# Optimization experiments

Measured on AMD Instinct MI355X. Metric: run time of the kernel, lower is better.

## Reference

```python
import jax, jax.numpy as jnp
import numpy as np

SIG = 0.5
EPSILON = 10.0
E = float(np.e)


def setup_inputs() -> dict:
    key = jax.random.key(0)
    k1, k2, k3, k4 = jax.random.split(key, 4)
    B, S, D, K = 8, 2048, 128, 64
    features = jax.random.normal(k1, (B, S, D), dtype=jnp.float32)
    centroids = jax.random.normal(k2, (K, D), dtype=jnp.float32)
    # phi are per-class scale stats; keep strictly positive
    phi = jax.random.uniform(k3, (K,), dtype=jnp.float32, minval=0.5, maxval=1.5)
    labels = jax.random.randint(k4, (B, S), 0, K, dtype=jnp.int32)
    return {"features": features, "centroids": centroids, "phi": phi, "labels": labels}


def _proto_supcon_loss(features, centroids, phi, labels):
    B, S, D = features.shape
    K = centroids.shape[0]
    # pairwise mean-squared-error (MSELoss reduction='mean' over D):
    # d2[b,i,j] = mean_d (f[b,i,d]-f[b,j,d])^2
    sq = jnp.sum(features * features, axis=-1)  # [B,S]
    gram = jnp.einsum('bid,bjd->bij', features, features)  # [B,S,S]
    d2 = (sq[:, :, None] + sq[:, None, :] - 2.0 * gram) / D
    d2 = jnp.maximum(d2, 0.0)

    same = labels[:, :, None] == labels[:, None, :]  # [B,S,S]
    neg_mask = ~same
    neg_cnt = jnp.sum(neg_mask, axis=-1)  # [B,S]
    # negative sample term: neg_x = mean over negatives of MSE; neg_sup = x*log(x+e)
    neg_x = jnp.sum(jnp.where(neg_mask, d2, 0.0), axis=-1) / jnp.maximum(neg_cnt, 1)
    neg_sup = neg_x * jnp.log(neg_x + E)

    # positive sample term: mean over same-label j != i (0 if no other positive,
    # matching pos_dis = [0] in the original)
    eye = jnp.eye(S, dtype=bool)
    pos_mask = same & ~eye
    pos_cnt = jnp.sum(pos_mask, axis=-1)
    pos_x = jnp.sum(jnp.where(pos_mask, d2, 0.0), axis=-1) / jnp.maximum(pos_cnt, 1)

    # centroid terms: MSE(feature, centroid_k)/phi_k, [B,S,K]
    csq = jnp.sum(centroids * centroids, axis=-1)  # [K]
    cgram = jnp.einsum('bsd,kd->bsk', features, centroids)
    cd2 = (sq[:, :, None] + csq[None, None, :] - 2.0 * cgram) / D
    cd2 = jnp.maximum(cd2, 0.0) / phi[None, None, :]

    pos_cent = jnp.take_along_axis(cd2, labels[:, :, None].astype(jnp.int32), axis=2)[..., 0]  # [B,S]
    neg_cent_x = (jnp.sum(cd2, axis=-1) - pos_cent) / (K - 1)
    neg_cent_log = neg_cent_x * jnp.log(neg_cent_x + E)

    pos_spcl = SIG * pos_x + (1.0 - SIG) * pos_cent
    neg_spcl = SIG * neg_sup + (1.0 - SIG) * neg_cent_log
    per_anchor = pos_spcl - neg_spcl + EPSILON

    # anchors contribute only if they have at least one negative sample
    contrib = neg_cnt > 0
    loss = jnp.sum(jnp.where(contrib, per_anchor, 0.0)) / S
    return loss.reshape(1, 1)


def reference(features, centroids, phi, labels):
    return _proto_supcon_loss(features, centroids, phi, labels)
```

## Files before the change

### kernel.cpp

```cpp
#include <hip/hip_runtime.h>
#include <math.h>

#define B_ 8
#define S_ 2048
#define D_ 128
#define K_ 64
#define SIG_ 0.5f
#define EPS_ 10.0f
#define E_ 2.718281828459045f

__device__ __forceinline__ int remap512(int bx) {
    return ((bx & 7) << 6) | (bx >> 3);
}

__global__ void __launch_bounds__(256) k1_stats(
    const float* __restrict__ F, const int* __restrict__ L,
    float* __restrict__ fsumK, float* __restrict__ ssumK, float* __restrict__ cntK) {
    int bx = remap512(blockIdx.x);
    int k = bx & (K_ - 1);
    int b = bx >> 6;
    int tid = threadIdx.x;
    int lane = tid & 63;
    int wv = tid >> 6;

    __shared__ float redF[4][128];
    __shared__ float redS[4];
    __shared__ int   redC[4];

    const int* Lb = L + b * S_;
    const float* Fb = F + (size_t)b * S_ * D_;

    float a0 = 0.f, a1 = 0.f, q0 = 0.f, q1 = 0.f;
    int cnt = 0;
    #pragma unroll
    for (int rr = 0; rr < 8; ++rr) {
        int r = (wv << 3) + rr;
        int lbl = Lb[(r << 6) + lane];
        unsigned long long m = __ballot(lbl == k);
        cnt += (int)__popcll(m);
        while (m) {
            int i = __ffsll((long long)m) - 1;
            m &= m - 1;
            const float* row = Fb + (size_t)((r << 6) + i) * D_;
            float v0 = row[lane];
            float v1 = row[64 + lane];
            a0 += v0; q0 = fmaf(v0, v0, q0);
            a1 += v1; q1 = fmaf(v1, v1, q1);
        }
    }
    float qq = q0 + q1;
    #pragma unroll
    for (int m = 1; m < 64; m <<= 1) qq += __shfl_xor(qq, m);
    redF[wv][lane] = a0;
    redF[wv][64 + lane] = a1;
    if (lane == 0) { redS[wv] = qq; redC[wv] = cnt; }
    __syncthreads();

    if (tid < 128) {
        float s = (redF[0][tid] + redF[1][tid]) + (redF[2][tid] + redF[3][tid]);
        fsumK[(size_t)bx * D_ + tid] = s;
    }
    if (tid == 0) {
        ssumK[bx] = (redS[0] + redS[1]) + (redS[2] + redS[3]);
        cntK[bx] = (float)(redC[0] + redC[1] + redC[2] + redC[3]);
    }
}

__global__ void __launch_bounds__(256) k3_main(
    const float* __restrict__ F, const float* __restrict__ C,
    const float* __restrict__ phi, const int* __restrict__ L,
    const float* __restrict__ fsumK, const float* __restrict__ ssumK,
    const float* __restrict__ cntK, float* __restrict__ partial) {

    __shared__ float Cs[K_ * 129];
    __shared__ float4 redA[256];
    __shared__ float Fa[D_];
    __shared__ float wacc[4];
    int tid = threadIdx.x;
    int bxw = remap512(blockIdx.x);
    int b = bxw >> 6;

    {
        const float4* C4 = (const float4*)C;
        #pragma unroll
        for (int it = 0; it < 8; ++it) {
            int i = it * 256 + tid;
            float4 v = C4[i];
            float* p = &Cs[(i >> 5) * 129 + ((i & 31) << 2)];
            p[0] = v.x; p[1] = v.y; p[2] = v.z; p[3] = v.w;
        }
    }
    {
        int d4 = tid & 31, kg = tid >> 5;
        const float4* g4 = (const float4*)(fsumK + (size_t)b * K_ * D_) + (size_t)kg * 8 * 32 + d4;
        float4 s; s.x = s.y = s.z = s.w = 0.f;
        #pragma unroll
        for (int kk = 0; kk < 8; ++kk) {
            float4 v = g4[(size_t)kk * 32];
            s.x += v.x; s.y += v.y; s.z += v.z; s.w += v.w;
        }
        redA[tid] = s;
    }
    __syncthreads();
    if (tid < 32) {
        float4 a; a.x = a.y = a.z = a.w = 0.f;
        #pragma unroll
        for (int g = 0; g < 8; ++g) {
            float4 v = redA[g * 32 + tid];
            a.x += v.x; a.y += v.y; a.z += v.z; a.w += v.w;
        }
        ((float4*)Fa)[tid] = a;
    }
    __syncthreads();

    int lane = tid & 63;

    float c0 = 0.f, c1 = 0.f, c2 = 0.f, c3 = 0.f;
    #pragma unroll
    for (int dd = 0; dd < D_; dd += 4) {
        c0 = fmaf(Cs[lane * 129 + dd + 0], Cs[lane * 129 + dd + 0], c0);
        c1 = fmaf(Cs[lane * 129 + dd + 1], Cs[lane * 129 + dd + 1], c1);
        c2 = fmaf(Cs[lane * 129 + dd + 2], Cs[lane * 129 + dd + 2], c2);
        c3 = fmaf(Cs[lane * 129 + dd + 3], Cs[lane * 129 + dd + 3], c3);
    }
    float csq = (c0 + c1) + (c2 + c3);
    float phv = phi[lane];
    float ssl = ssumK[b * K_ + lane];
    float cnl = cntK[b * K_ + lane];
    float ssA = ssl;
    #pragma unroll
    for (int m = 1; m < 64; m <<= 1) ssA += __shfl_xor(ssA, m);

    int wid = __builtin_amdgcn_readfirstlane(tid) >> 6;
    int o = bxw * 4 + wid;
    int a0g = o * 8;
    const float4* F4 = (const float4*)F;

    int j_of = lane >> 3, q = lane & 7;
    int a_mine = a0g + j_of;
    int lbl_p = L[a_mine];
    const float4* fr = F4 + (size_t)a_mine * 32;
    const float4* fk = (const float4*)(fsumK + (size_t)(b * K_ + lbl_p) * D_);
    const float4* fa4 = (const float4*)Fa;

    float sq_p = 0.f, dk_p = 0.f, da_p = 0.f;
    #pragma unroll
    for (int i = 0; i < 4; ++i) {
        int dq = i * 8 + q;
        float4 fv = fr[dq];
        float4 kv = fk[dq];
        float4 av = fa4[dq];
        sq_p = fmaf(fv.x, fv.x, fmaf(fv.y, fv.y, fmaf(fv.z, fv.z, fmaf(fv.w, fv.w, sq_p))));
        dk_p = fmaf(fv.x, kv.x, fmaf(fv.y, kv.y, fmaf(fv.z, kv.z, fmaf(fv.w, kv.w, dk_p))));
        da_p = fmaf(fv.x, av.x, fmaf(fv.y, av.y, fmaf(fv.z, av.z, fmaf(fv.w, av.w, da_p))));
    }
    #pragma unroll
    for (int m = 1; m < 8; m <<= 1) {
        sq_p += __shfl_xor(sq_p, m);
        dk_p += __shfl_xor(dk_p, m);
        da_p += __shfl_xor(da_p, m);
    }

    float facc[8];
    #pragma unroll
    for (int j = 0; j < 8; ++j) facc[j] = 0.f;

    float4 fw[8], fwn[8];
    #pragma unroll
    for (int j = 0; j < 8; ++j) fw[j] = F4[(size_t)(a0g + j) * 32 + 0];

    for (int dq = 0; dq < 32; ++dq) {
        if (dq < 31) {
            #pragma unroll
            for (int j = 0; j < 8; ++j) fwn[j] = F4[(size_t)(a0g + j) * 32 + dq + 1];
        }
        int cbase = lane * 129 + (dq << 2);
        #pragma unroll
        for (int l = 0; l < 4; ++l) {
            float cs = Cs[cbase + l];
            #pragma unroll
            for (int j = 0; j < 8; ++j) {
                float fe = (l == 0) ? fw[j].x : (l == 1) ? fw[j].y : (l == 2) ? fw[j].z : fw[j].w;
                facc[j] = fmaf(fe, cs, facc[j]);
            }
        }
        #pragma unroll
        for (int j = 0; j < 8; ++j) fw[j] = fwn[j];
    }

    float acc = 0.f;
    #pragma unroll
    for (int j = 0; j < 8; ++j) {
        float sq_j = __shfl(sq_p, j * 8);
        float dk_j = __shfl(dk_p, j * 8);
        float da_j = __shfl(da_p, j * 8);
        int lbl_j = __shfl(lbl_p, j * 8);
        float cnt_j = __shfl(cnl, lbl_j);
        float ssm_j = __shfl(ssl, lbl_j);

        float cd2 = (sq_j + csq - 2.f * facc[j]) * (1.f / D_);
        cd2 = fmaxf(cd2, 0.f) / phv;

        float s_cd = cd2;
        #pragma unroll
        for (int m = 1; m < 64; m <<= 1) s_cd += __shfl_xor(s_cd, m);
        float pos_cent = __shfl(cd2, lbl_j);

        float ncx = (s_cd - pos_cent) * (1.f / (K_ - 1));
        float S_same = (cnt_j * sq_j + ssm_j - 2.f * dk_j) * (1.f / D_);
        float S_all = ((float)S_ * sq_j + ssA - 2.f * da_j) * (1.f / D_);
        float pos_x = fmaxf(S_same, 0.f) / fmaxf(cnt_j - 1.f, 1.f);
        float neg_cnt = (float)S_ - cnt_j;
        float neg_x = fmaxf(S_all - S_same, 0.f) / fmaxf(neg_cnt, 1.f);

        float neg_sup = neg_x * __logf(neg_x + E_);
        float ncl = ncx * __logf(ncx + E_);

        float pa = SIG_ * pos_x + (1.f - SIG_) * pos_cent
                 - (SIG_ * neg_sup + (1.f - SIG_) * ncl) + EPS_;
        if (neg_cnt > 0.5f) acc += pa;
    }

    if (lane == 0) wacc[wid] = acc;
    __syncthreads();

    if (tid == 0) partial[bxw] = wacc[0] + wacc[1] + wacc[2] + wacc[3];
}

__global__ void __launch_bounds__(256) k4_reduce(
    const float* __restrict__ partial, float* __restrict__ out) {
    int tid = threadIdx.x;
    int lane = tid & 63;
    int wv = tid >> 6;
    __shared__ float w[4];
    float v = partial[tid] + partial[tid + 256];
    #pragma unroll
    for (int m = 1; m < 64; m <<= 1) v += __shfl_xor(v, m);
    if (lane == 0) w[wv] = v;
    __syncthreads();
    if (tid == 0) out[0] = (w[0] + w[1] + w[2] + w[3]) * (1.0f / (float)S_);
}

extern "C" void kernel_launch(void* const* d_in, const int* in_sizes, int n_in,
                              void* d_out, int out_size, void* d_ws, size_t ws_size,
                              hipStream_t stream) {
    const float* F = (const float*)d_in[0];
    const float* C = (const float*)d_in[1];
    const float* phi = (const float*)d_in[2];
    const int* L = (const int*)d_in[3];
    float* out = (float*)d_out;

    float* ws = (float*)d_ws;
    float* fsumK = ws;
    float* ssumK = fsumK + (size_t)B_ * K_ * D_;
    float* cntK  = ssumK + B_ * K_;
    float* partial = cntK + B_ * K_;

    k1_stats<<<B_ * K_, 256, 0, stream>>>(F, L, fsumK, ssumK, cntK);
    k3_main<<<512, 256, 0, stream>>>(F, C, phi, L, fsumK, ssumK, cntK, partial);
    k4_reduce<<<1, 256, 0, stream>>>(partial, out);
}
```

Measured before the change: 28.05 us.

## Use 512-thread main blocks and precompute centroid norms in stats kernel

The main kernel now runs 256 blocks of 512 threads instead of 512 blocks of 256, so each block's centroid staging into shared memory and its fsumK prefix reduction serve twice as many anchor waves. The squared centroid norms are computed once in the stats kernel and stored in workspace, rather than being recomputed from shared memory in every block. The final reduction reads 256 partials. Fewer, larger blocks may lower occupancy or leave some of the MI355X's CUs idle.

```diff
diff --git a/kernel.cpp b/kernel.cpp
--- a/kernel.cpp
+++ b/kernel.cpp
@@ -9,13 +9,14 @@
 #define EPS_ 10.0f
 #define E_ 2.718281828459045f
 
-__device__ __forceinline__ int remap512(int bx) {
-    return ((bx & 7) << 6) | (bx >> 3);
-}
+__device__ __forceinline__ int remap512(int bx) { return ((bx & 7) << 6) | (bx >> 3); }
+__device__ __forceinline__ int remap256(int bx) { return ((bx & 7) << 5) | (bx >> 3); }
 
 __global__ void __launch_bounds__(256) k1_stats(
-    const float* __restrict__ F, const int* __restrict__ L,
-    float* __restrict__ fsumK, float* __restrict__ ssumK, float* __restrict__ cntK) {
+    const float* __restrict__ F, const float* __restrict__ C,
+    const int* __restrict__ L,
+    float* __restrict__ fsumK, float* __restrict__ ssumK, float* __restrict__ cntK,
+    float* __restrict__ csqK) {
     int bx = remap512(blockIdx.x);
     int k = bx & (K_ - 1);
     int b = bx >> 6;
@@ -64,33 +65,42 @@
         ssumK[bx] = (redS[0] + redS[1]) + (redS[2] + redS[3]);
         cntK[bx] = (float)(redC[0] + redC[1] + redC[2] + redC[3]);
     }
-}
-
-__global__ void __launch_bounds__(256) k3_main(
+    if (b == 0 && wv == 0) {
+        float x0 = C[(k << 7) + lane];
+        float x1 = C[(k << 7) + 64 + lane];
+        float cs = fmaf(x0, x0, x1 * x1);
+        #pragma unroll
+        for (int m = 1; m < 64; m <<= 1) cs += __shfl_xor(cs, m);
+        if (lane == 0) csqK[k] = cs;
+    }
+}
+
+__global__ void __launch_bounds__(512) k3_main(
     const float* __restrict__ F, const float* __restrict__ C,
     const float* __restrict__ phi, const int* __restrict__ L,
     const float* __restrict__ fsumK, const float* __restrict__ ssumK,
-    const float* __restrict__ cntK, float* __restrict__ partial) {
+    const float* __restrict__ cntK, const float* __restrict__ csqK,
+    float* __restrict__ partial) {
 
     __shared__ float Cs[K_ * 129];
     __shared__ float4 redA[256];
     __shared__ float Fa[D_];
-    __shared__ float wacc[4];
+    __shared__ float wacc[8];
     int tid = threadIdx.x;
-    int bxw = remap512(blockIdx.x);
-    int b = bxw >> 6;
+    int bxw = remap256(blockIdx.x);
+    int b = bxw >> 5;
 
     {
         const float4* C4 = (const float4*)C;
         #pragma unroll
-        for (int it = 0; it < 8; ++it) {
-            int i = it * 256 + tid;
+        for (int it = 0; it < 4; ++it) {
+            int i = it * 512 + tid;
             float4 v = C4[i];
             float* p = &Cs[(i >> 5) * 129 + ((i & 31) << 2)];
             p[0] = v.x; p[1] = v.y; p[2] = v.z; p[3] = v.w;
         }
     }
-    {
+    if (tid < 256) {
         int d4 = tid & 31, kg = tid >> 5;
         const float4* g4 = (const float4*)(fsumK + (size_t)b * K_ * D_) + (size_t)kg * 8 * 32 + d4;
         float4 s; s.x = s.y = s.z = s.w = 0.f;
@@ -115,15 +125,7 @@
 
     int lane = tid & 63;
 
-    float c0 = 0.f, c1 = 0.f, c2 = 0.f, c3 = 0.f;
-    #pragma unroll
-    for (int dd = 0; dd < D_; dd += 4) {
-        c0 = fmaf(Cs[lane * 129 + dd + 0], Cs[lane * 129 + dd + 0], c0);
-        c1 = fmaf(Cs[lane * 129 + dd + 1], Cs[lane * 129 + dd + 1], c1);
-        c2 = fmaf(Cs[lane * 129 + dd + 2], Cs[lane * 129 + dd + 2], c2);
-        c3 = fmaf(Cs[lane * 129 + dd + 3], Cs[lane * 129 + dd + 3], c3);
-    }
-    float csq = (c0 + c1) + (c2 + c3);
+    float csq = csqK[lane];
     float phv = phi[lane];
     float ssl = ssumK[b * K_ + lane];
     float cnl = cntK[b * K_ + lane];
@@ -132,7 +134,7 @@
     for (int m = 1; m < 64; m <<= 1) ssA += __shfl_xor(ssA, m);
 
     int wid = __builtin_amdgcn_readfirstlane(tid) >> 6;
-    int o = bxw * 4 + wid;
+    int o = bxw * 8 + wid;
     int a0g = o * 8;
     const float4* F4 = (const float4*)F;
 
@@ -224,7 +226,12 @@
     if (lane == 0) wacc[wid] = acc;
     __syncthreads();
 
-    if (tid == 0) partial[bxw] = wacc[0] + wacc[1] + wacc[2] + wacc[3];
+    if (tid == 0) {
+        float s = 0.f;
+        #pragma unroll
+        for (int w = 0; w < 8; ++w) s += wacc[w];
+        partial[bxw] = s;
+    }
 }
 
 __global__ void __launch_bounds__(256) k4_reduce(
@@ -233,7 +240,7 @@
     int lane = tid & 63;
     int wv = tid >> 6;
     __shared__ float w[4];
-    float v = partial[tid] + partial[tid + 256];
+    float v = partial[tid];
     #pragma unroll
     for (int m = 1; m < 64; m <<= 1) v += __shfl_xor(v, m);
     if (lane == 0) w[wv] = v;
@@ -254,9 +261,10 @@
     float* fsumK = ws;
     float* ssumK = fsumK + (size_t)B_ * K_ * D_;
     float* cntK  = ssumK + B_ * K_;
-    float* partial = cntK + B_ * K_;
-
-    k1_stats<<<B_ * K_, 256, 0, stream>>>(F, L, fsumK, ssumK, cntK);
-    k3_main<<<512, 256, 0, stream>>>(F, C, phi, L, fsumK, ssumK, cntK, partial);
+    float* csqK  = cntK + B_ * K_;
+    float* partial = csqK + K_;
+
+    k1_stats<<<B_ * K_, 256, 0, stream>>>(F, C, L, fsumK, ssumK, cntK, csqK);
+    k3_main<<<256, 512, 0, stream>>>(F, C, phi, L, fsumK, ssumK, cntK, csqK, partial);
     k4_reduce<<<1, 256, 0, stream>>>(partial, out);
 }
```

After: 27.00 us. -3.8%, faster.
